# Kernel optimization log

Hardware: AMD Instinct MI355X
Metric: run time of the kernel (lower is better)

Reference implementation:

```python
import jax, jax.numpy as jnp
import numpy as np

B, S, H, L, D, DI = 4, 32, 8, 128, 512, 2048
EPS = 1e-6
TEMP = float(D) ** 0.5


def layer_norm(x, g, b):
    mu = jnp.mean(x, axis=-1, keepdims=True)
    var = jnp.mean((x - mu) ** 2, axis=-1, keepdims=True)
    return (x - mu) * jax.lax.rsqrt(var + EPS) * g + b


def setup_inputs() -> dict:
    key = jax.random.key(0)
    ks = jax.random.split(key, 8)
    x = jax.random.normal(ks[0], (B, S, L, D), jnp.float32)
    mask = jax.random.randint(ks[1], (B, S, L), 0, 2, jnp.int32)
    # learned params
    w = jax.random.normal(ks[2], (1, 1, H, L, D), jnp.float32) * (1.0 / np.sqrt(D))
    v_w = jax.random.normal(ks[3], (D, D), jnp.float32) * 0.02   # nn.Linear weight (out,in)
    ln_g = jnp.ones((D,), jnp.float32)
    ln_b = jnp.zeros((D,), jnp.float32)
    w1 = jax.random.normal(ks[4], (DI, D), jnp.float32) * 0.02
    b1 = jnp.zeros((DI,), jnp.float32)
    w2 = jax.random.normal(ks[5], (D, DI), jnp.float32) * 0.02
    b2 = jnp.zeros((D,), jnp.float32)
    fln_g = jnp.ones((D,), jnp.float32)
    fln_b = jnp.zeros((D,), jnp.float32)
    return {"x": x, "mask": mask, "w": w, "v_w": v_w, "ln_g": ln_g, "ln_b": ln_b,
            "w1": w1, "b1": b1, "w2": w2, "b2": b2, "fln_g": fln_g, "fln_b": fln_b}


def reference(x, mask, w, v_w, ln_g, ln_b, w1, b1, w2, b2, fln_g, fln_b):
    # attn logits: broadcast mul + reduce over d_model == einsum over d
    attn = jnp.einsum('bsld,hld->bshl', x, w[0, 0]) / TEMP           # (B,S,H,L)
    attn = jnp.where(mask[:, :, None, :] == 0, -1e9, attn)
    attn = jax.nn.softmax(attn, axis=-1)                              # dropout: eval mode
    v = jnp.einsum('bsld,ed->bsle', x, v_w)                           # Linear no bias: x @ W.T
    out = jnp.einsum('bsld,bshl->bshd', v, attn)                      # weighted sum readout
    out = layer_norm(out, ln_g, ln_b)
    # PositionwiseFeedForward with residual + LayerNorm
    h = jax.nn.relu(jnp.einsum('bshd,fd->bshf', out, w1) + b1)
    y = jnp.einsum('bshf,df->bshd', h, w2) + b2 + out
    y = layer_norm(y, fln_g, fln_b)
    return y, attn
```

## Files before the change

kernel.cpp:

```cpp
#include <hip/hip_runtime.h>
#include <hip/hip_bf16.h>

#define BB 4
#define SS 32
#define HH 8
#define LL 128
#define DD 512
#define DI 2048
#define EPSN 1e-6f
#define INV_TEMP 0.04419417382415922f

#define NLOGW_BLK 512
#define NCAST_GRAN ((DI*DD/4)*2 + (DD*DD/4))
#define NCAST_BLK (NCAST_GRAN / 256)

#define NROW (BB*SS*HH)
#define SLICE ((size_t)NROW * DD)
#define NAVL_BLK 64

typedef __attribute__((ext_vector_type(8))) short short8;
typedef __attribute__((ext_vector_type(4))) float float4v;

static __device__ __forceinline__ unsigned short f2b(float f) {
  __hip_bfloat16 h = __float2bfloat16(f);
  return *(unsigned short*)&h;
}

static __device__ __forceinline__ size_t pk(int m, int k, int K) {
  return ((((size_t)(m >> 4) * (K >> 5) + (k >> 5)) * 4 + ((k >> 3) & 3)) * 16
          + (m & 15)) * 8 + (k & 7);
}

__global__ __launch_bounds__(256) void pre_kernel(
    const float* __restrict__ x, const int* __restrict__ mask,
    const float* __restrict__ w, const float* __restrict__ w1,
    const float* __restrict__ w2, const float* __restrict__ v_w,
    unsigned short* __restrict__ w1b, unsigned short* __restrict__ w2b,
    unsigned short* __restrict__ v_wb, float* __restrict__ logits) {
  int blk = blockIdx.x;
  if (blk < NLOGW_BLK) {
    int wv = threadIdx.x >> 6, lane = threadIdx.x & 63;
    int p   = blk * 4 + wv;
    int l   = p >> 4;
    int bsg = p & 15;

    float4 wr[HH][2];
#pragma unroll
    for (int h = 0; h < HH; ++h) {
      const float4* wp = (const float4*)(w + ((size_t)h * LL + l) * DD) + lane * 2;
      wr[h][0] = wp[0];
      wr[h][1] = wp[1];
    }

#pragma unroll 2
    for (int i = 0; i < 8; ++i) {
      int bs = bsg * 8 + i;
      const float4* xr = (const float4*)(x + ((size_t)bs * LL + l) * DD) + lane * 2;
      float4 x0 = xr[0], x1 = xr[1];
      float acc[HH];
#pragma unroll
      for (int h = 0; h < HH; ++h) {
        acc[h] = x0.x * wr[h][0].x + x0.y * wr[h][0].y +
                 x0.z * wr[h][0].z + x0.w * wr[h][0].w +
                 x1.x * wr[h][1].x + x1.y * wr[h][1].y +
                 x1.z * wr[h][1].z + x1.w * wr[h][1].w;
      }
#pragma unroll
      for (int off = 32; off > 0; off >>= 1) {
#pragma unroll
        for (int h = 0; h < HH; ++h) acc[h] += __shfl_xor(acc[h], off);
      }
      if (lane == 0) {
        int msk = mask[bs * LL + l];
#pragma unroll
        for (int h = 0; h < HH; ++h) {
          float lg = msk ? acc[h] * INV_TEMP : -1e9f;
          logits[((size_t)bs * HH + h) * LL + l] = lg;
        }
      }
    }
  } else {
    const int n1 = (DI * DD) / 4;
    const int n2 = n1;
    int i = (blk - NLOGW_BLK) * 256 + threadIdx.x;
    float4 v;
    unsigned short* dst;
    size_t base;
    if (i < n1) {
      v = ((const float4*)w1)[i];
      dst = w1b;
      base = pk(i >> 7, (i & 127) * 4, DD);
    } else if (i < n1 + n2) {
      int j = i - n1;
      v = ((const float4*)w2)[j];
      dst = w2b;
      base = pk(j >> 9, (j & 511) * 4, DI);
    } else {
      int j = i - n1 - n2;
      v = ((const float4*)v_w)[j];
      dst = v_wb;
      base = pk(j >> 7, (j & 127) * 4, DD);
    }
    dst[base + 0] = f2b(v.x);
    dst[base + 1] = f2b(v.y);
    dst[base + 2] = f2b(v.z);
    dst[base + 3] = f2b(v.w);
  }
}

__global__ __launch_bounds__(512) void attn_v_ln_kernel(
    const float* __restrict__ x, const float* __restrict__ logits,
    const unsigned short* __restrict__ v_wb, const float* __restrict__ ln_g,
    const float* __restrict__ ln_b, float* __restrict__ attn_out,
    float* __restrict__ o_ln, unsigned short* __restrict__ o_lnb) {
  int blk = blockIdx.x;
  int t = threadIdx.x, wv = t >> 6, lane = t & 63;
  int bs0 = blk * 2;

  __shared__ __align__(16) float sattnT[LL][20];
  __shared__ __align__(16) unsigned short apk[16 * DD];
  __shared__ float wstat[8][16][2];
  __shared__ float rstat[16][2];

#pragma unroll
  for (int rr = 0; rr < 2; ++rr) {
    int r = wv * 2 + rr;
    int bs = bs0 + (r >> 3), h = r & 7;
    const float* lg = logits + ((size_t)bs * HH + h) * LL;
    float v0 = lg[lane], v1 = lg[lane + 64];
    float m = fmaxf(v0, v1);
#pragma unroll
    for (int off = 32; off > 0; off >>= 1) m = fmaxf(m, __shfl_xor(m, off));
    float e0 = __expf(v0 - m), e1 = __expf(v1 - m);
    float s = e0 + e1;
#pragma unroll
    for (int off = 32; off > 0; off >>= 1) s += __shfl_xor(s, off);
    float inv = 1.f / s;
    e0 *= inv; e1 *= inv;
    sattnT[lane][r]      = e0;
    sattnT[lane + 64][r] = e1;
    float* ao = attn_out + ((size_t)bs * HH + h) * LL;
    ao[lane]      = e0;
    ao[lane + 64] = e1;
  }
  __syncthreads();

  {
    int e = t;
    const float* xb = x + (size_t)bs0 * LL * DD + e;
    float acc[16];
#pragma unroll
    for (int m = 0; m < 16; ++m) acc[m] = 0.f;
#pragma unroll 2
    for (int l = 0; l < LL; l += 4) {
      float xv0[4], xv1[4];
#pragma unroll
      for (int j = 0; j < 4; ++j) {
        xv0[j] = xb[(size_t)(l + j) * DD];
        xv1[j] = xb[(size_t)(LL + l + j) * DD];
      }
#pragma unroll
      for (int j = 0; j < 4; ++j) {
        float4 a0 = *(const float4*)&sattnT[l + j][0];
        float4 a1 = *(const float4*)&sattnT[l + j][4];
        float4 a2 = *(const float4*)&sattnT[l + j][8];
        float4 a3 = *(const float4*)&sattnT[l + j][12];
        acc[0]  += a0.x * xv0[j]; acc[1]  += a0.y * xv0[j];
        acc[2]  += a0.z * xv0[j]; acc[3]  += a0.w * xv0[j];
        acc[4]  += a1.x * xv0[j]; acc[5]  += a1.y * xv0[j];
        acc[6]  += a1.z * xv0[j]; acc[7]  += a1.w * xv0[j];
        acc[8]  += a2.x * xv1[j]; acc[9]  += a2.y * xv1[j];
        acc[10] += a2.z * xv1[j]; acc[11] += a2.w * xv1[j];
        acc[12] += a3.x * xv1[j]; acc[13] += a3.y * xv1[j];
        acc[14] += a3.z * xv1[j]; acc[15] += a3.w * xv1[j];
      }
    }
    unsigned base = ((e >> 5) * 4 + ((e >> 3) & 3)) * 128 + (e & 7);
#pragma unroll
    for (int m = 0; m < 16; ++m) apk[base + m * 8] = f2b(acc[m]);
  }
  __syncthreads();

  int lm = lane & 15, lq = lane >> 4;
  int n0 = wv * 64;
  const short8* A8 = (const short8*)apk;
  const short8* B8 = (const short8*)v_wb;
  float4v acc3[4];
#pragma unroll
  for (int nf = 0; nf < 4; ++nf) acc3[nf] = (float4v){0.f, 0.f, 0.f, 0.f};
#pragma unroll 4
  for (int c = 0; c < 16; ++c) {
    short8 a = A8[c * 64 + lane];
#pragma unroll
    for (int nf = 0; nf < 4; ++nf) {
      short8 b = B8[((size_t)((n0 >> 4) + nf) * 16 + c) * 64 + lane];
      acc3[nf] = __builtin_amdgcn_mfma_f32_16x16x32_bf16(a, b, acc3[nf], 0, 0, 0);
    }
  }

  float srow[4], qrow[4];
#pragma unroll
  for (int r = 0; r < 4; ++r) {
    float s = 0.f, q = 0.f;
#pragma unroll
    for (int nf = 0; nf < 4; ++nf) { float v = acc3[nf][r]; s += v; q += v * v; }
#pragma unroll
    for (int off = 1; off < 16; off <<= 1) {
      s += __shfl_xor(s, off);
      q += __shfl_xor(q, off);
    }
    srow[r] = s; qrow[r] = q;
  }
  if (lm == 0) {
#pragma unroll
    for (int r = 0; r < 4; ++r) {
      wstat[wv][lq * 4 + r][0] = srow[r];
      wstat[wv][lq * 4 + r][1] = qrow[r];
    }
  }
  __syncthreads();
  if (t < 16) {
    float S = 0.f, Q = 0.f;
#pragma unroll
    for (int w8 = 0; w8 < 8; ++w8) { S += wstat[w8][t][0]; Q += wstat[w8][t][1]; }
    float mu  = S * (1.f / DD);
    float var = Q * (1.f / DD) - mu * mu;
    rstat[t][0] = mu;
    rstat[t][1] = rsqrtf(var + EPSN);
  }
  __syncthreads();
#pragma unroll
  for (int nf = 0; nf < 4; ++nf) {
    int col = n0 + nf * 16 + lm;
    float g = ln_g[col], bcol = ln_b[col];
#pragma unroll
    for (int r = 0; r < 4; ++r) {
      int row = lq * 4 + r;
      float v = (acc3[nf][r] - rstat[row][0]) * rstat[row][1] * g + bcol;
      int grow = blk * 16 + row;
      o_ln[(size_t)grow * DD + col] = v;
      o_lnb[pk(grow, col, DD)] = f2b(v);
    }
  }
}

__global__ __launch_bounds__(256) void gemm1_kernel(
    const unsigned short* __restrict__ o_lnb, const unsigned short* __restrict__ w1b,
    const float* __restrict__ b1, unsigned short* __restrict__ h1b) {
  int blk = blockIdx.x;
  int nt = blk & 31, mt = blk >> 5;
  int wv = threadIdx.x >> 6, lane = threadIdx.x & 63;
  int lm = lane & 15, lq = lane >> 4;

  int m0 = mt * 64 + wv * 16;
  int n0 = nt * 64;
  const short8* A8 = (const short8*)o_lnb + (size_t)(m0 >> 4) * 16 * 64;
  const short8* B8 = (const short8*)w1b;

  float4v acc[4];
#pragma unroll
  for (int nf = 0; nf < 4; ++nf) acc[nf] = (float4v){0.f, 0.f, 0.f, 0.f};

#pragma unroll 4
  for (int c = 0; c < 16; ++c) {
    short8 a = A8[(size_t)c * 64 + lane];
#pragma unroll
    for (int nf = 0; nf < 4; ++nf) {
      short8 b = B8[((size_t)((n0 >> 4) + nf) * 16 + c) * 64 + lane];
      acc[nf] = __builtin_amdgcn_mfma_f32_16x16x32_bf16(a, b, acc[nf], 0, 0, 0);
    }
  }

#pragma unroll
  for (int nf = 0; nf < 4; ++nf) {
    int col = n0 + nf * 16 + lm;
    float bb = b1[col];
#pragma unroll
    for (int r = 0; r < 4; ++r) {
      int row = m0 + lq * 4 + r;
      h1b[pk(row, col, DI)] = f2b(fmaxf(acc[nf][r] + bb, 0.f));
    }
  }
}

__global__ __launch_bounds__(256) void gemm2_kernel(
    const unsigned short* __restrict__ h1b, const unsigned short* __restrict__ w2b,
    float* __restrict__ ypart) {
  int blk = blockIdx.x;
  int nt = blk & 7, mt = (blk >> 3) & 15, kslice = blk >> 7;
  int wv = threadIdx.x >> 6, lane = threadIdx.x & 63;
  int lm = lane & 15, lq = lane >> 4;

  int m0 = mt * 64 + wv * 16;
  int n0 = nt * 64;
  const short8* A8 = (const short8*)h1b + (size_t)(m0 >> 4) * 64 * 64;
  const short8* B8 = (const short8*)w2b;

  float4v acc[4];
#pragma unroll
  for (int nf = 0; nf < 4; ++nf) acc[nf] = (float4v){0.f, 0.f, 0.f, 0.f};

#pragma unroll 4
  for (int ci = 0; ci < 16; ++ci) {
    int c = kslice * 16 + ci;
    short8 a = A8[(size_t)c * 64 + lane];
#pragma unroll
    for (int nf = 0; nf < 4; ++nf) {
      short8 b = B8[((size_t)((n0 >> 4) + nf) * 64 + c) * 64 + lane];
      acc[nf] = __builtin_amdgcn_mfma_f32_16x16x32_bf16(a, b, acc[nf], 0, 0, 0);
    }
  }

  float* outp = ypart + (size_t)kslice * SLICE;
#pragma unroll
  for (int nf = 0; nf < 4; ++nf) {
    int col = n0 + nf * 16 + lm;
#pragma unroll
    for (int r = 0; r < 4; ++r)
      outp[(size_t)(m0 + lq * 4 + r) * DD + col] = acc[nf][r];
  }
}

__global__ __launch_bounds__(256) void ln_final_kernel(
    const float* __restrict__ ypart, const float* __restrict__ o_ln,
    const float* __restrict__ b2, const float* __restrict__ fln_g,
    const float* __restrict__ fln_b, float* __restrict__ y_out) {
  int wv = threadIdx.x >> 6, lane = threadIdx.x & 63;
  int row = blockIdx.x * 4 + wv;

  const float* p0 = ypart + (size_t)row * DD;
  const float* ol = o_ln + (size_t)row * DD;
  float vals[8];
  float sum = 0.f, sq = 0.f;
#pragma unroll
  for (int k = 0; k < 8; ++k) {
    int d = lane + 64 * k;
    float v = p0[d] + p0[SLICE + d] + p0[2 * SLICE + d] + p0[3 * SLICE + d] +
              b2[d] + ol[d];
    vals[k] = v;
    sum += v;
    sq += v * v;
  }
#pragma unroll
  for (int off = 32; off > 0; off >>= 1) {
    sum += __shfl_xor(sum, off);
    sq  += __shfl_xor(sq, off);
  }
  float mu  = sum * (1.f / DD);
  float var = sq * (1.f / DD) - mu * mu;
  float rs  = rsqrtf(var + EPSN);
  float* yo = y_out + (size_t)row * DD;
#pragma unroll
  for (int k = 0; k < 8; ++k) {
    int d = lane + 64 * k;
    yo[d] = (vals[k] - mu) * rs * fln_g[d] + fln_b[d];
  }
}

extern "C" void kernel_launch(void* const* d_in, const int* in_sizes, int n_in,
                              void* d_out, int out_size, void* d_ws, size_t ws_size,
                              hipStream_t stream) {
  const float* x     = (const float*)d_in[0];
  const int*   mask  = (const int*)d_in[1];
  const float* w     = (const float*)d_in[2];
  const float* v_w   = (const float*)d_in[3];
  const float* ln_g  = (const float*)d_in[4];
  const float* ln_b  = (const float*)d_in[5];
  const float* w1    = (const float*)d_in[6];
  const float* b1    = (const float*)d_in[7];
  const float* w2    = (const float*)d_in[8];
  const float* b2    = (const float*)d_in[9];
  const float* fln_g = (const float*)d_in[10];
  const float* fln_b = (const float*)d_in[11];

  float* y    = (float*)d_out;
  float* attn = y + (size_t)BB * SS * HH * DD;

  char* ws = (char*)d_ws;
  float*          o_ln   = (float*)(ws);
  unsigned short* o_lnb  = (unsigned short*)(ws + 2097152);
  unsigned short* w1b    = (unsigned short*)(ws + 3145728);
  unsigned short* w2b    = (unsigned short*)(ws + 5242880);
  unsigned short* h1b    = (unsigned short*)(ws + 7340032);
  float*          ypart  = (float*)(ws + 11534336);
  unsigned short* v_wb   = (unsigned short*)(ws + 19922944);
  float*          logits = (float*)(ws + 29884416);

  pre_kernel<<<NLOGW_BLK + NCAST_BLK, 256, 0, stream>>>(
      x, mask, w, w1, w2, v_w, w1b, w2b, v_wb, logits);
  attn_v_ln_kernel<<<NAVL_BLK, 512, 0, stream>>>(
      x, logits, v_wb, ln_g, ln_b, attn, o_ln, o_lnb);
  gemm1_kernel<<<512, 256, 0, stream>>>(o_lnb, w1b, b1, h1b);
  gemm2_kernel<<<512, 256, 0, stream>>>(h1b, w2b, ypart);
  ln_final_kernel<<<256, 256, 0, stream>>>(ypart, o_ln, b2, fln_g, fln_b, y);
}
```

Baseline: 156.2 us.

## Fuse all stages into one persistent kernel with software grid barriers

Replaces the five separate kernel launches with one persistent 256-block kernel. Stages are separated by atomic-counter grid barriers, and the counters are zeroed by a memset before the launch. The attention readout is split per (bs, 64-column) tile across more blocks. The second GEMM is no longer split along K, so the final LayerNorm is fused into its epilogue and the partial-sum buffer goes away. This removes launch gaps and the intermediate round trip, at the cost of barrier spin time, fewer active blocks in the GEMM2 and V-projection stages (64 of 256), and reliance on all blocks being co-resident.

```diff
diff --git a/kernel.cpp b/kernel.cpp
--- a/kernel.cpp
+++ b/kernel.cpp
@@ -10,13 +10,9 @@
 #define EPSN 1e-6f
 #define INV_TEMP 0.04419417382415922f
 
-#define NLOGW_BLK 512
 #define NCAST_GRAN ((DI*DD/4)*2 + (DD*DD/4))
-#define NCAST_BLK (NCAST_GRAN / 256)
-
 #define NROW (BB*SS*HH)
-#define SLICE ((size_t)NROW * DD)
-#define NAVL_BLK 64
+#define GRID 256
 
 typedef __attribute__((ext_vector_type(8))) short short8;
 typedef __attribute__((ext_vector_type(4))) float float4v;
@@ -31,19 +27,44 @@
           + (m & 15)) * 8 + (k & 7);
 }
 
-__global__ __launch_bounds__(256) void pre_kernel(
+static __device__ __forceinline__ void gbar(unsigned* ctr) {
+  __syncthreads();
+  if (threadIdx.x == 0) {
+    __threadfence();
+    atomicAdd(ctr, 1u);
+    while (__hip_atomic_load(ctr, __ATOMIC_ACQUIRE, __HIP_MEMORY_SCOPE_AGENT) <
+           (unsigned)GRID)
+      __builtin_amdgcn_s_sleep(2);
+    __threadfence();
+  }
+  __syncthreads();
+}
+
+__global__ __launch_bounds__(256) void fused_all(
     const float* __restrict__ x, const int* __restrict__ mask,
-    const float* __restrict__ w, const float* __restrict__ w1,
-    const float* __restrict__ w2, const float* __restrict__ v_w,
+    const float* __restrict__ w, const float* __restrict__ v_w,
+    const float* __restrict__ ln_g, const float* __restrict__ ln_b,
+    const float* __restrict__ w1, const float* __restrict__ b1,
+    const float* __restrict__ w2, const float* __restrict__ b2,
+    const float* __restrict__ fln_g, const float* __restrict__ fln_b,
     unsigned short* __restrict__ w1b, unsigned short* __restrict__ w2b,
-    unsigned short* __restrict__ v_wb, float* __restrict__ logits) {
-  int blk = blockIdx.x;
-  if (blk < NLOGW_BLK) {
-    int wv = threadIdx.x >> 6, lane = threadIdx.x & 63;
-    int p   = blk * 4 + wv;
-    int l   = p >> 4;
-    int bsg = p & 15;
-
+    unsigned short* __restrict__ v_wb, float* __restrict__ logits,
+    unsigned short* __restrict__ xab, float* __restrict__ o_ln,
+    unsigned short* __restrict__ o_lnb, unsigned short* __restrict__ h1b,
+    float* __restrict__ attn_out, float* __restrict__ y_out,
+    unsigned* __restrict__ bar) {
+  int t = threadIdx.x, wv = t >> 6, lane = t & 63;
+  int gw = blockIdx.x * 4 + wv;
+  const int NWAVE = GRID * 4;
+  int lm = lane & 15, lq = lane >> 4;
+
+  __shared__ __align__(16) float sattnT[LL * 12];
+  __shared__ float sxa[4][HH][64];
+  __shared__ float wstat[4][16][2];
+  __shared__ float rstat[16][2];
+
+  for (int p = gw; p < 2048; p += NWAVE) {
+    int l = p >> 4, bsg = p & 15;
     float4 wr[HH][2];
 #pragma unroll
     for (int h = 0; h < HH; ++h) {
@@ -51,7 +72,6 @@
       wr[h][0] = wp[0];
       wr[h][1] = wp[1];
     }
-
 #pragma unroll 2
     for (int i = 0; i < 8; ++i) {
       int bs = bsg * 8 + i;
@@ -79,281 +99,260 @@
         }
       }
     }
-  } else {
+  }
+  {
     const int n1 = (DI * DD) / 4;
     const int n2 = n1;
-    int i = (blk - NLOGW_BLK) * 256 + threadIdx.x;
-    float4 v;
-    unsigned short* dst;
-    size_t base;
-    if (i < n1) {
-      v = ((const float4*)w1)[i];
-      dst = w1b;
-      base = pk(i >> 7, (i & 127) * 4, DD);
-    } else if (i < n1 + n2) {
-      int j = i - n1;
-      v = ((const float4*)w2)[j];
-      dst = w2b;
-      base = pk(j >> 9, (j & 511) * 4, DI);
-    } else {
-      int j = i - n1 - n2;
-      v = ((const float4*)v_w)[j];
-      dst = v_wb;
-      base = pk(j >> 7, (j & 127) * 4, DD);
-    }
-    dst[base + 0] = f2b(v.x);
-    dst[base + 1] = f2b(v.y);
-    dst[base + 2] = f2b(v.z);
-    dst[base + 3] = f2b(v.w);
-  }
-}
-
-__global__ __launch_bounds__(512) void attn_v_ln_kernel(
-    const float* __restrict__ x, const float* __restrict__ logits,
-    const unsigned short* __restrict__ v_wb, const float* __restrict__ ln_g,
-    const float* __restrict__ ln_b, float* __restrict__ attn_out,
-    float* __restrict__ o_ln, unsigned short* __restrict__ o_lnb) {
-  int blk = blockIdx.x;
-  int t = threadIdx.x, wv = t >> 6, lane = t & 63;
-  int bs0 = blk * 2;
-
-  __shared__ __align__(16) float sattnT[LL][20];
-  __shared__ __align__(16) unsigned short apk[16 * DD];
-  __shared__ float wstat[8][16][2];
-  __shared__ float rstat[16][2];
-
-#pragma unroll
-  for (int rr = 0; rr < 2; ++rr) {
-    int r = wv * 2 + rr;
-    int bs = bs0 + (r >> 3), h = r & 7;
-    const float* lg = logits + ((size_t)bs * HH + h) * LL;
-    float v0 = lg[lane], v1 = lg[lane + 64];
-    float m = fmaxf(v0, v1);
-#pragma unroll
-    for (int off = 32; off > 0; off >>= 1) m = fmaxf(m, __shfl_xor(m, off));
-    float e0 = __expf(v0 - m), e1 = __expf(v1 - m);
-    float s = e0 + e1;
-#pragma unroll
-    for (int off = 32; off > 0; off >>= 1) s += __shfl_xor(s, off);
-    float inv = 1.f / s;
-    e0 *= inv; e1 *= inv;
-    sattnT[lane][r]      = e0;
-    sattnT[lane + 64][r] = e1;
-    float* ao = attn_out + ((size_t)bs * HH + h) * LL;
-    ao[lane]      = e0;
-    ao[lane + 64] = e1;
-  }
-  __syncthreads();
-
-  {
-    int e = t;
-    const float* xb = x + (size_t)bs0 * LL * DD + e;
-    float acc[16];
-#pragma unroll
-    for (int m = 0; m < 16; ++m) acc[m] = 0.f;
-#pragma unroll 2
-    for (int l = 0; l < LL; l += 4) {
-      float xv0[4], xv1[4];
-#pragma unroll
-      for (int j = 0; j < 4; ++j) {
-        xv0[j] = xb[(size_t)(l + j) * DD];
-        xv1[j] = xb[(size_t)(LL + l + j) * DD];
-      }
-#pragma unroll
-      for (int j = 0; j < 4; ++j) {
-        float4 a0 = *(const float4*)&sattnT[l + j][0];
-        float4 a1 = *(const float4*)&sattnT[l + j][4];
-        float4 a2 = *(const float4*)&sattnT[l + j][8];
-        float4 a3 = *(const float4*)&sattnT[l + j][12];
-        acc[0]  += a0.x * xv0[j]; acc[1]  += a0.y * xv0[j];
-        acc[2]  += a0.z * xv0[j]; acc[3]  += a0.w * xv0[j];
-        acc[4]  += a1.x * xv0[j]; acc[5]  += a1.y * xv0[j];
-        acc[6]  += a1.z * xv0[j]; acc[7]  += a1.w * xv0[j];
-        acc[8]  += a2.x * xv1[j]; acc[9]  += a2.y * xv1[j];
-        acc[10] += a2.z * xv1[j]; acc[11] += a2.w * xv1[j];
-        acc[12] += a3.x * xv1[j]; acc[13] += a3.y * xv1[j];
-        acc[14] += a3.z * xv1[j]; acc[15] += a3.w * xv1[j];
-      }
-    }
-    unsigned base = ((e >> 5) * 4 + ((e >> 3) & 3)) * 128 + (e & 7);
-#pragma unroll
-    for (int m = 0; m < 16; ++m) apk[base + m * 8] = f2b(acc[m]);
-  }
-  __syncthreads();
-
-  int lm = lane & 15, lq = lane >> 4;
-  int n0 = wv * 64;
-  const short8* A8 = (const short8*)apk;
-  const short8* B8 = (const short8*)v_wb;
-  float4v acc3[4];
-#pragma unroll
-  for (int nf = 0; nf < 4; ++nf) acc3[nf] = (float4v){0.f, 0.f, 0.f, 0.f};
+    int tid = blockIdx.x * 256 + t;
+    const int NT = GRID * 256;
+    for (int i = tid; i < NCAST_GRAN; i += NT) {
+      float4 v;
+      unsigned short* dst;
+      size_t base;
+      if (i < n1) {
+        v = ((const float4*)w1)[i];
+        dst = w1b;
+        base = pk(i >> 7, (i & 127) * 4, DD);
+      } else if (i < n1 + n2) {
+        int j = i - n1;
+        v = ((const float4*)w2)[j];
+        dst = w2b;
+        base = pk(j >> 9, (j & 511) * 4, DI);
+      } else {
+        int j = i - n1 - n2;
+        v = ((const float4*)v_w)[j];
+        dst = v_wb;
+        base = pk(j >> 7, (j & 127) * 4, DD);
+      }
+      dst[base + 0] = f2b(v.x);
+      dst[base + 1] = f2b(v.y);
+      dst[base + 2] = f2b(v.z);
+      dst[base + 3] = f2b(v.w);
+    }
+  }
+  gbar(bar + 0);
+
+  for (int bt = blockIdx.x; bt < 1024; bt += GRID) {
+    int bs = bt >> 3, eo = (bt & 7) << 6;
+#pragma unroll
+    for (int rr = 0; rr < 2; ++rr) {
+      int h = wv * 2 + rr;
+      const float* lg = logits + ((size_t)bs * HH + h) * LL;
+      float v0 = lg[lane], v1 = lg[lane + 64];
+      float m = fmaxf(v0, v1);
+#pragma unroll
+      for (int off = 32; off > 0; off >>= 1) m = fmaxf(m, __shfl_xor(m, off));
+      float e0 = __expf(v0 - m), e1 = __expf(v1 - m);
+      float s = e0 + e1;
+#pragma unroll
+      for (int off = 32; off > 0; off >>= 1) s += __shfl_xor(s, off);
+      float inv = 1.f / s;
+      e0 *= inv; e1 *= inv;
+      sattnT[lane * 12 + h]        = e0;
+      sattnT[(lane + 64) * 12 + h] = e1;
+      if ((bt & 7) == 0) {
+        float* ao = attn_out + ((size_t)bs * HH + h) * LL;
+        ao[lane]      = e0;
+        ao[lane + 64] = e1;
+      }
+    }
+    __syncthreads();
+    {
+      int el = t & 63, lseg = t >> 6;
+      int e = eo + el;
+      const float* xb = x + (size_t)bs * LL * DD + e;
+      float acc[HH];
+#pragma unroll
+      for (int h = 0; h < HH; ++h) acc[h] = 0.f;
+      int l0 = lseg * 32;
 #pragma unroll 4
-  for (int c = 0; c < 16; ++c) {
-    short8 a = A8[c * 64 + lane];
+      for (int l = l0; l < l0 + 32; ++l) {
+        float xv = xb[(size_t)l * DD];
+        float4 a0 = *(const float4*)&sattnT[l * 12];
+        float4 a1 = *(const float4*)&sattnT[l * 12 + 4];
+        acc[0] += a0.x * xv; acc[1] += a0.y * xv;
+        acc[2] += a0.z * xv; acc[3] += a0.w * xv;
+        acc[4] += a1.x * xv; acc[5] += a1.y * xv;
+        acc[6] += a1.z * xv; acc[7] += a1.w * xv;
+      }
+#pragma unroll
+      for (int h = 0; h < HH; ++h) sxa[lseg][h][el] = acc[h];
+    }
+    __syncthreads();
+    for (int o = t; o < 512; o += 256) {
+      int h = o >> 6, el2 = o & 63;
+      float v = sxa[0][h][el2] + sxa[1][h][el2] + sxa[2][h][el2] + sxa[3][h][el2];
+      xab[pk(bs * HH + h, eo + el2, DD)] = f2b(v);
+    }
+    __syncthreads();
+  }
+  gbar(bar + 1);
+
+  if (blockIdx.x < 64) {
+    int mt = blockIdx.x;
+    const short8* A8 = (const short8*)xab + (size_t)mt * 16 * 64;
+    const short8* B8 = (const short8*)v_wb;
+    int n0 = wv * 128;
+    float4v acc[8];
+#pragma unroll
+    for (int nf = 0; nf < 8; ++nf) acc[nf] = (float4v){0.f, 0.f, 0.f, 0.f};
+#pragma unroll 4
+    for (int c = 0; c < 16; ++c) {
+      short8 a = A8[c * 64 + lane];
+#pragma unroll
+      for (int nf = 0; nf < 8; ++nf) {
+        short8 b = B8[((size_t)(wv * 8 + nf) * 16 + c) * 64 + lane];
+        acc[nf] = __builtin_amdgcn_mfma_f32_16x16x32_bf16(a, b, acc[nf], 0, 0, 0);
+      }
+    }
+    float srow[4], qrow[4];
+#pragma unroll
+    for (int r = 0; r < 4; ++r) {
+      float s = 0.f, q = 0.f;
+#pragma unroll
+      for (int nf = 0; nf < 8; ++nf) { float v = acc[nf][r]; s += v; q += v * v; }
+#pragma unroll
+      for (int off = 1; off < 16; off <<= 1) {
+        s += __shfl_xor(s, off);
+        q += __shfl_xor(q, off);
+      }
+      srow[r] = s; qrow[r] = q;
+    }
+    if (lm == 0) {
+#pragma unroll
+      for (int r = 0; r < 4; ++r) {
+        wstat[wv][lq * 4 + r][0] = srow[r];
+        wstat[wv][lq * 4 + r][1] = qrow[r];
+      }
+    }
+    __syncthreads();
+    if (t < 16) {
+      float S = 0.f, Q = 0.f;
+#pragma unroll
+      for (int w4 = 0; w4 < 4; ++w4) { S += wstat[w4][t][0]; Q += wstat[w4][t][1]; }
+      float mu  = S * (1.f / DD);
+      float var = Q * (1.f / DD) - mu * mu;
+      rstat[t][0] = mu;
+      rstat[t][1] = rsqrtf(var + EPSN);
+    }
+    __syncthreads();
+#pragma unroll
+    for (int nf = 0; nf < 8; ++nf) {
+      int col = n0 + nf * 16 + lm;
+      float g = ln_g[col], bcol = ln_b[col];
+#pragma unroll
+      for (int r = 0; r < 4; ++r) {
+        int row = lq * 4 + r;
+        float v = (acc[nf][r] - rstat[row][0]) * rstat[row][1] * g + bcol;
+        int grow = mt * 16 + row;
+        o_ln[(size_t)grow * DD + col] = v;
+        o_lnb[pk(grow, col, DD)] = f2b(v);
+      }
+    }
+  }
+  gbar(bar + 2);
+
+  for (int wt = gw; wt < 2048; wt += NWAVE) {
+    int nt = wt & 31, mt = wt >> 5;
+    const short8* A8 = (const short8*)o_lnb + (size_t)mt * 16 * 64;
+    const short8* B8 = (const short8*)w1b;
+    float4v acc1[4];
+#pragma unroll
+    for (int nf = 0; nf < 4; ++nf) acc1[nf] = (float4v){0.f, 0.f, 0.f, 0.f};
+#pragma unroll 4
+    for (int c = 0; c < 16; ++c) {
+      short8 a = A8[c * 64 + lane];
+#pragma unroll
+      for (int nf = 0; nf < 4; ++nf) {
+        short8 b = B8[((size_t)(nt * 4 + nf) * 16 + c) * 64 + lane];
+        acc1[nf] = __builtin_amdgcn_mfma_f32_16x16x32_bf16(a, b, acc1[nf], 0, 0, 0);
+      }
+    }
+    int m0 = mt * 16, n0 = nt * 64;
 #pragma unroll
     for (int nf = 0; nf < 4; ++nf) {
-      short8 b = B8[((size_t)((n0 >> 4) + nf) * 16 + c) * 64 + lane];
-      acc3[nf] = __builtin_amdgcn_mfma_f32_16x16x32_bf16(a, b, acc3[nf], 0, 0, 0);
-    }
-  }
-
-  float srow[4], qrow[4];
-#pragma unroll
-  for (int r = 0; r < 4; ++r) {
-    float s = 0.f, q = 0.f;
-#pragma unroll
-    for (int nf = 0; nf < 4; ++nf) { float v = acc3[nf][r]; s += v; q += v * v; }
-#pragma unroll
-    for (int off = 1; off < 16; off <<= 1) {
-      s += __shfl_xor(s, off);
-      q += __shfl_xor(q, off);
-    }
-    srow[r] = s; qrow[r] = q;
-  }
-  if (lm == 0) {
+      int col = n0 + nf * 16 + lm;
+      float bb = b1[col];
+#pragma unroll
+      for (int r = 0; r < 4; ++r) {
+        int row = m0 + lq * 4 + r;
+        h1b[pk(row, col, DI)] = f2b(fmaxf(acc1[nf][r] + bb, 0.f));
+      }
+    }
+  }
+  gbar(bar + 3);
+
+  if (blockIdx.x < 64) {
+    int mt = blockIdx.x;
+    const short8* A8 = (const short8*)h1b + (size_t)mt * 64 * 64;
+    const short8* B8 = (const short8*)w2b;
+    int n0 = wv * 128;
+    float4v acc[8];
+#pragma unroll
+    for (int nf = 0; nf < 8; ++nf) acc[nf] = (float4v){0.f, 0.f, 0.f, 0.f};
+#pragma unroll 4
+    for (int c = 0; c < 64; ++c) {
+      short8 a = A8[c * 64 + lane];
+#pragma unroll
+      for (int nf = 0; nf < 8; ++nf) {
+        short8 b = B8[((size_t)(wv * 8 + nf) * 64 + c) * 64 + lane];
+        acc[nf] = __builtin_amdgcn_mfma_f32_16x16x32_bf16(a, b, acc[nf], 0, 0, 0);
+      }
+    }
+    float vals[8][4];
+#pragma unroll
+    for (int nf = 0; nf < 8; ++nf) {
+      int col = n0 + nf * 16 + lm;
+      float bb = b2[col];
+#pragma unroll
+      for (int r = 0; r < 4; ++r) {
+        int grow = mt * 16 + lq * 4 + r;
+        vals[nf][r] = acc[nf][r] + bb + o_ln[(size_t)grow * DD + col];
+      }
+    }
+    float srow[4], qrow[4];
 #pragma unroll
     for (int r = 0; r < 4; ++r) {
-      wstat[wv][lq * 4 + r][0] = srow[r];
-      wstat[wv][lq * 4 + r][1] = qrow[r];
-    }
-  }
-  __syncthreads();
-  if (t < 16) {
-    float S = 0.f, Q = 0.f;
-#pragma unroll
-    for (int w8 = 0; w8 < 8; ++w8) { S += wstat[w8][t][0]; Q += wstat[w8][t][1]; }
-    float mu  = S * (1.f / DD);
-    float var = Q * (1.f / DD) - mu * mu;
-    rstat[t][0] = mu;
-    rstat[t][1] = rsqrtf(var + EPSN);
-  }
-  __syncthreads();
-#pragma unroll
-  for (int nf = 0; nf < 4; ++nf) {
-    int col = n0 + nf * 16 + lm;
-    float g = ln_g[col], bcol = ln_b[col];
-#pragma unroll
-    for (int r = 0; r < 4; ++r) {
-      int row = lq * 4 + r;
-      float v = (acc3[nf][r] - rstat[row][0]) * rstat[row][1] * g + bcol;
-      int grow = blk * 16 + row;
-      o_ln[(size_t)grow * DD + col] = v;
-      o_lnb[pk(grow, col, DD)] = f2b(v);
-    }
-  }
-}
-
-__global__ __launch_bounds__(256) void gemm1_kernel(
-    const unsigned short* __restrict__ o_lnb, const unsigned short* __restrict__ w1b,
-    const float* __restrict__ b1, unsigned short* __restrict__ h1b) {
-  int blk = blockIdx.x;
-  int nt = blk & 31, mt = blk >> 5;
-  int wv = threadIdx.x >> 6, lane = threadIdx.x & 63;
-  int lm = lane & 15, lq = lane >> 4;
-
-  int m0 = mt * 64 + wv * 16;
-  int n0 = nt * 64;
-  const short8* A8 = (const short8*)o_lnb + (size_t)(m0 >> 4) * 16 * 64;
-  const short8* B8 = (const short8*)w1b;
-
-  float4v acc[4];
-#pragma unroll
-  for (int nf = 0; nf < 4; ++nf) acc[nf] = (float4v){0.f, 0.f, 0.f, 0.f};
-
-#pragma unroll 4
-  for (int c = 0; c < 16; ++c) {
-    short8 a = A8[(size_t)c * 64 + lane];
-#pragma unroll
-    for (int nf = 0; nf < 4; ++nf) {
-      short8 b = B8[((size_t)((n0 >> 4) + nf) * 16 + c) * 64 + lane];
-      acc[nf] = __builtin_amdgcn_mfma_f32_16x16x32_bf16(a, b, acc[nf], 0, 0, 0);
-    }
-  }
-
-#pragma unroll
-  for (int nf = 0; nf < 4; ++nf) {
-    int col = n0 + nf * 16 + lm;
-    float bb = b1[col];
-#pragma unroll
-    for (int r = 0; r < 4; ++r) {
-      int row = m0 + lq * 4 + r;
-      h1b[pk(row, col, DI)] = f2b(fmaxf(acc[nf][r] + bb, 0.f));
-    }
-  }
-}
-
-__global__ __launch_bounds__(256) void gemm2_kernel(
-    const unsigned short* __restrict__ h1b, const unsigned short* __restrict__ w2b,
-    float* __restrict__ ypart) {
-  int blk = blockIdx.x;
-  int nt = blk & 7, mt = (blk >> 3) & 15, kslice = blk >> 7;
-  int wv = threadIdx.x >> 6, lane = threadIdx.x & 63;
-  int lm = lane & 15, lq = lane >> 4;
-
-  int m0 = mt * 64 + wv * 16;
-  int n0 = nt * 64;
-  const short8* A8 = (const short8*)h1b + (size_t)(m0 >> 4) * 64 * 64;
-  const short8* B8 = (const short8*)w2b;
-
-  float4v acc[4];
-#pragma unroll
-  for (int nf = 0; nf < 4; ++nf) acc[nf] = (float4v){0.f, 0.f, 0.f, 0.f};
-
-#pragma unroll 4
-  for (int ci = 0; ci < 16; ++ci) {
-    int c = kslice * 16 + ci;
-    short8 a = A8[(size_t)c * 64 + lane];
-#pragma unroll
-    for (int nf = 0; nf < 4; ++nf) {
-      short8 b = B8[((size_t)((n0 >> 4) + nf) * 64 + c) * 64 + lane];
-      acc[nf] = __builtin_amdgcn_mfma_f32_16x16x32_bf16(a, b, acc[nf], 0, 0, 0);
-    }
-  }
-
-  float* outp = ypart + (size_t)kslice * SLICE;
-#pragma unroll
-  for (int nf = 0; nf < 4; ++nf) {
-    int col = n0 + nf * 16 + lm;
-#pragma unroll
-    for (int r = 0; r < 4; ++r)
-      outp[(size_t)(m0 + lq * 4 + r) * DD + col] = acc[nf][r];
-  }
-}
-
-__global__ __launch_bounds__(256) void ln_final_kernel(
-    const float* __restrict__ ypart, const float* __restrict__ o_ln,
-    const float* __restrict__ b2, const float* __restrict__ fln_g,
-    const float* __restrict__ fln_b, float* __restrict__ y_out) {
-  int wv = threadIdx.x >> 6, lane = threadIdx.x & 63;
-  int row = blockIdx.x * 4 + wv;
-
-  const float* p0 = ypart + (size_t)row * DD;
-  const float* ol = o_ln + (size_t)row * DD;
-  float vals[8];
-  float sum = 0.f, sq = 0.f;
-#pragma unroll
-  for (int k = 0; k < 8; ++k) {
-    int d = lane + 64 * k;
-    float v = p0[d] + p0[SLICE + d] + p0[2 * SLICE + d] + p0[3 * SLICE + d] +
-              b2[d] + ol[d];
-    vals[k] = v;
-    sum += v;
-    sq += v * v;
-  }
-#pragma unroll
-  for (int off = 32; off > 0; off >>= 1) {
-    sum += __shfl_xor(sum, off);
-    sq  += __shfl_xor(sq, off);
-  }
-  float mu  = sum * (1.f / DD);
-  float var = sq * (1.f / DD) - mu * mu;
-  float rs  = rsqrtf(var + EPSN);
-  float* yo = y_out + (size_t)row * DD;
-#pragma unroll
-  for (int k = 0; k < 8; ++k) {
-    int d = lane + 64 * k;
-    yo[d] = (vals[k] - mu) * rs * fln_g[d] + fln_b[d];
+      float s = 0.f, q = 0.f;
+#pragma unroll
+      for (int nf = 0; nf < 8; ++nf) { float v = vals[nf][r]; s += v; q += v * v; }
+#pragma unroll
+      for (int off = 1; off < 16; off <<= 1) {
+        s += __shfl_xor(s, off);
+        q += __shfl_xor(q, off);
+      }
+      srow[r] = s; qrow[r] = q;
+    }
+    if (lm == 0) {
+#pragma unroll
+      for (int r = 0; r < 4; ++r) {
+        wstat[wv][lq * 4 + r][0] = srow[r];
+        wstat[wv][lq * 4 + r][1] = qrow[r];
+      }
+    }
+    __syncthreads();
+    if (t < 16) {
+      float S = 0.f, Q = 0.f;
+#pragma unroll
+      for (int w4 = 0; w4 < 4; ++w4) { S += wstat[w4][t][0]; Q += wstat[w4][t][1]; }
+      float mu  = S * (1.f / DD);
+      float var = Q * (1.f / DD) - mu * mu;
+      rstat[t][0] = mu;
+      rstat[t][1] = rsqrtf(var + EPSN);
+    }
+    __syncthreads();
+#pragma unroll
+    for (int nf = 0; nf < 8; ++nf) {
+      int col = n0 + nf * 16 + lm;
+      float g = fln_g[col], bcol = fln_b[col];
+#pragma unroll
+      for (int r = 0; r < 4; ++r) {
+        int row = lq * 4 + r;
+        int grow = mt * 16 + row;
+        y_out[(size_t)grow * DD + col] =
+            (vals[nf][r] - rstat[row][0]) * rstat[row][1] * g + bcol;
+      }
+    }
   }
 }
 
@@ -382,15 +381,13 @@
   unsigned short* w1b    = (unsigned short*)(ws + 3145728);
   unsigned short* w2b    = (unsigned short*)(ws + 5242880);
   unsigned short* h1b    = (unsigned short*)(ws + 7340032);
-  float*          ypart  = (float*)(ws + 11534336);
   unsigned short* v_wb   = (unsigned short*)(ws + 19922944);
+  unsigned short* xab    = (unsigned short*)(ws + 20447232);
   float*          logits = (float*)(ws + 29884416);
-
-  pre_kernel<<<NLOGW_BLK + NCAST_BLK, 256, 0, stream>>>(
-      x, mask, w, w1, w2, v_w, w1b, w2b, v_wb, logits);
-  attn_v_ln_kernel<<<NAVL_BLK, 512, 0, stream>>>(
-      x, logits, v_wb, ln_g, ln_b, attn, o_ln, o_lnb);
-  gemm1_kernel<<<512, 256, 0, stream>>>(o_lnb, w1b, b1, h1b);
-  gemm2_kernel<<<512, 256, 0, stream>>>(h1b, w2b, ypart);
-  ln_final_kernel<<<256, 256, 0, stream>>>(ypart, o_ln, b2, fln_g, fln_b, y);
-}
+  unsigned*       bar    = (unsigned*)(ws + 33554432);
+
+  hipMemsetAsync(bar, 0, 64, stream);
+  fused_all<<<GRID, 256, 0, stream>>>(
+      x, mask, w, v_w, ln_g, ln_b, w1, b1, w2, b2, fln_g, fln_b,
+      w1b, w2b, v_wb, logits, xab, o_ln, o_lnb, h1b, attn, y, bar);
+}
```

After: 500.9 us. 3.21x slower.

## Fuse second FFN GEMM with residual and final LayerNorm, drop split-K

Applied to the files above, without the earlier changes.

Replaces the split-K gemm2 kernel (512 blocks writing four fp32 partial slices) and the separate final LayerNorm kernel with one kernel. Each 512-thread block computes a full 16-row by 512-column tile over the whole K=2048 and does bias, residual, and LayerNorm in-register with shared-memory row statistics. This removes the partial-sum buffer round trip and one launch. In exchange only 64 blocks run on a GPU with many more CUs, and each wave has a 4x longer serial K loop, so parallelism drops sharply.

```diff
diff --git a/kernel.cpp b/kernel.cpp
--- a/kernel.cpp
+++ b/kernel.cpp
@@ -15,7 +15,6 @@
 #define NCAST_BLK (NCAST_GRAN / 256)
 
 #define NROW (BB*SS*HH)
-#define SLICE ((size_t)NROW * DD)
 #define NAVL_BLK 64
 
 typedef __attribute__((ext_vector_type(8))) short short8;
@@ -283,17 +282,20 @@
   }
 }
 
-__global__ __launch_bounds__(256) void gemm2_kernel(
+__global__ __launch_bounds__(512) void gemm2_ln_kernel(
     const unsigned short* __restrict__ h1b, const unsigned short* __restrict__ w2b,
-    float* __restrict__ ypart) {
-  int blk = blockIdx.x;
-  int nt = blk & 7, mt = (blk >> 3) & 15, kslice = blk >> 7;
-  int wv = threadIdx.x >> 6, lane = threadIdx.x & 63;
+    const float* __restrict__ o_ln, const float* __restrict__ b2,
+    const float* __restrict__ fln_g, const float* __restrict__ fln_b,
+    float* __restrict__ y_out) {
+  int mt = blockIdx.x;
+  int t = threadIdx.x, wv = t >> 6, lane = t & 63;
   int lm = lane & 15, lq = lane >> 4;
-
-  int m0 = mt * 64 + wv * 16;
-  int n0 = nt * 64;
-  const short8* A8 = (const short8*)h1b + (size_t)(m0 >> 4) * 64 * 64;
+  int n0 = wv * 64;
+
+  __shared__ float wstat[8][16][2];
+  __shared__ float rstat[16][2];
+
+  const short8* A8 = (const short8*)h1b + (size_t)mt * 64 * 64;
   const short8* B8 = (const short8*)w2b;
 
   float4v acc[4];
@@ -301,8 +303,7 @@
   for (int nf = 0; nf < 4; ++nf) acc[nf] = (float4v){0.f, 0.f, 0.f, 0.f};
 
 #pragma unroll 4
-  for (int ci = 0; ci < 16; ++ci) {
-    int c = kslice * 16 + ci;
+  for (int c = 0; c < 64; ++c) {
     short8 a = A8[(size_t)c * 64 + lane];
 #pragma unroll
     for (int nf = 0; nf < 4; ++nf) {
@@ -311,49 +312,60 @@
     }
   }
 
-  float* outp = ypart + (size_t)kslice * SLICE;
+  float vals[4][4];
 #pragma unroll
   for (int nf = 0; nf < 4; ++nf) {
     int col = n0 + nf * 16 + lm;
-#pragma unroll
-    for (int r = 0; r < 4; ++r)
-      outp[(size_t)(m0 + lq * 4 + r) * DD + col] = acc[nf][r];
-  }
-}
-
-__global__ __launch_bounds__(256) void ln_final_kernel(
-    const float* __restrict__ ypart, const float* __restrict__ o_ln,
-    const float* __restrict__ b2, const float* __restrict__ fln_g,
-    const float* __restrict__ fln_b, float* __restrict__ y_out) {
-  int wv = threadIdx.x >> 6, lane = threadIdx.x & 63;
-  int row = blockIdx.x * 4 + wv;
-
-  const float* p0 = ypart + (size_t)row * DD;
-  const float* ol = o_ln + (size_t)row * DD;
-  float vals[8];
-  float sum = 0.f, sq = 0.f;
-#pragma unroll
-  for (int k = 0; k < 8; ++k) {
-    int d = lane + 64 * k;
-    float v = p0[d] + p0[SLICE + d] + p0[2 * SLICE + d] + p0[3 * SLICE + d] +
-              b2[d] + ol[d];
-    vals[k] = v;
-    sum += v;
-    sq += v * v;
-  }
-#pragma unroll
-  for (int off = 32; off > 0; off >>= 1) {
-    sum += __shfl_xor(sum, off);
-    sq  += __shfl_xor(sq, off);
-  }
-  float mu  = sum * (1.f / DD);
-  float var = sq * (1.f / DD) - mu * mu;
-  float rs  = rsqrtf(var + EPSN);
-  float* yo = y_out + (size_t)row * DD;
-#pragma unroll
-  for (int k = 0; k < 8; ++k) {
-    int d = lane + 64 * k;
-    yo[d] = (vals[k] - mu) * rs * fln_g[d] + fln_b[d];
+    float bb = b2[col];
+#pragma unroll
+    for (int r = 0; r < 4; ++r) {
+      int grow = mt * 16 + lq * 4 + r;
+      vals[nf][r] = acc[nf][r] + bb + o_ln[(size_t)grow * DD + col];
+    }
+  }
+
+  float srow[4], qrow[4];
+#pragma unroll
+  for (int r = 0; r < 4; ++r) {
+    float s = 0.f, q = 0.f;
+#pragma unroll
+    for (int nf = 0; nf < 4; ++nf) { float v = vals[nf][r]; s += v; q += v * v; }
+#pragma unroll
+    for (int off = 1; off < 16; off <<= 1) {
+      s += __shfl_xor(s, off);
+      q += __shfl_xor(q, off);
+    }
+    srow[r] = s; qrow[r] = q;
+  }
+  if (lm == 0) {
+#pragma unroll
+    for (int r = 0; r < 4; ++r) {
+      wstat[wv][lq * 4 + r][0] = srow[r];
+      wstat[wv][lq * 4 + r][1] = qrow[r];
+    }
+  }
+  __syncthreads();
+  if (t < 16) {
+    float S = 0.f, Q = 0.f;
+#pragma unroll
+    for (int w8 = 0; w8 < 8; ++w8) { S += wstat[w8][t][0]; Q += wstat[w8][t][1]; }
+    float mu  = S * (1.f / DD);
+    float var = Q * (1.f / DD) - mu * mu;
+    rstat[t][0] = mu;
+    rstat[t][1] = rsqrtf(var + EPSN);
+  }
+  __syncthreads();
+#pragma unroll
+  for (int nf = 0; nf < 4; ++nf) {
+    int col = n0 + nf * 16 + lm;
+    float g = fln_g[col], bcol = fln_b[col];
+#pragma unroll
+    for (int r = 0; r < 4; ++r) {
+      int row = lq * 4 + r;
+      int grow = mt * 16 + row;
+      y_out[(size_t)grow * DD + col] =
+          (vals[nf][r] - rstat[row][0]) * rstat[row][1] * g + bcol;
+    }
   }
 }
 
@@ -382,7 +394,6 @@
   unsigned short* w1b    = (unsigned short*)(ws + 3145728);
   unsigned short* w2b    = (unsigned short*)(ws + 5242880);
   unsigned short* h1b    = (unsigned short*)(ws + 7340032);
-  float*          ypart  = (float*)(ws + 11534336);
   unsigned short* v_wb   = (unsigned short*)(ws + 19922944);
   float*          logits = (float*)(ws + 29884416);
 
@@ -391,6 +402,5 @@
   attn_v_ln_kernel<<<NAVL_BLK, 512, 0, stream>>>(
       x, logits, v_wb, ln_g, ln_b, attn, o_ln, o_lnb);
   gemm1_kernel<<<512, 256, 0, stream>>>(o_lnb, w1b, b1, h1b);
-  gemm2_kernel<<<512, 256, 0, stream>>>(h1b, w2b, ypart);
-  ln_final_kernel<<<256, 256, 0, stream>>>(ypart, o_ln, b2, fln_g, fln_b, y);
-}
+  gemm2_ln_kernel<<<64, 512, 0, stream>>>(h1b, w2b, o_ln, b2, fln_g, fln_b, y);
+}
```

After: 190.1 us. 1.22x slower.
